# Optimization experiments

Measured on AMD Instinct MI355X. Metric: run time of the kernel, lower is better.

## Reference

```python
import jax, jax.numpy as jnp
import numpy as np

EPS = 1e-7  # Keras backend epsilon


def setup_inputs() -> dict:
    key = jax.random.key(0)
    kx, ka, ke, kp = jax.random.split(key, 4)
    B, N, F, K_, C = 8, 2048, 128, 128, 128
    X = jax.random.normal(kx, (B, N, F), dtype=jnp.float32)
    Au = (jax.random.uniform(ka, (B, N, N)) < 0.05).astype(jnp.float32)
    A = jnp.maximum(Au, jnp.swapaxes(Au, -1, -2))
    W_emb = jax.random.normal(ke, (F, C), dtype=jnp.float32) * 0.1
    W_pool = jax.random.normal(kp, (F, K_), dtype=jnp.float32) * 0.1
    return {"X": X, "A": A, "W_emb": W_emb, "W_pool": W_pool}


def _diffpool(X, A, W_emb, W_pool):
    N = A.shape[-1]
    I = jnp.eye(N, dtype=A.dtype)
    A_ = A + I
    # symmetric normalization D^-1/2 (A+I) D^-1/2
    d = jax.lax.rsqrt(jnp.sum(A_, axis=-1))          # [B, N]
    fltr = A_ * d[..., :, None] * d[..., None, :]    # [B, N, N]

    Z = jnp.einsum('bnm,bmc->bnc', fltr, X @ W_emb)  # embedding GNN (no activation)
    S = jax.nn.softmax(jnp.einsum('bnm,bmk->bnk', fltr, X @ W_pool), axis=-1)  # [B, N, k]

    # link prediction loss: ||A - S S^T||_F per graph, mean over batch
    S_gram = jnp.einsum('bnk,bmk->bnm', S, S)
    LP_loss = jnp.mean(jnp.linalg.norm(A - S_gram, ord='fro', axis=(-1, -2)))

    # entropy loss on assignments
    entr = -jnp.sum(S * jnp.log(S + EPS), axis=-1)   # [B, N]
    entr_loss = jnp.mean(entr)

    X_pooled = jnp.einsum('bnk,bnc->bkc', S, Z)                  # S^T Z
    A_pooled = jnp.einsum('bnk,bnm,bml->bkl', S, A, S)           # S^T A S
    return X_pooled, A_pooled, S, LP_loss, entr_loss


def reference(X, A, W_emb, W_pool):
    return _diffpool(X, A, W_emb, W_pool)
```

## Files before the change

### kernel.cpp

```cpp
#include <hip/hip_runtime.h>
#include <math.h>

typedef __bf16 bf16x8 __attribute__((ext_vector_type(8)));
typedef float  f32x4  __attribute__((ext_vector_type(4)));
typedef unsigned short u16x4 __attribute__((ext_vector_type(4)));

#define DEVI __device__ __forceinline__

static constexpr int NB  = 8;
static constexpr int NN  = 2048;
static constexpr int NF  = 128;
static constexpr int NC2 = 256;

static constexpr int OUT_X0  = 0;
static constexpr int OUT_A0  = NB * 128 * 128;
static constexpr int OUT_S0  = OUT_A0 + NB * 128 * 128;
static constexpr int OUT_LP  = OUT_S0 + NB * NN * 128;
static constexpr int OUT_ENT = OUT_LP + 1;

DEVI unsigned short f2b(float f) {
  unsigned int u = __builtin_bit_cast(unsigned int, f);
  u += 0x7fffu + ((u >> 16) & 1u);
  return (unsigned short)(u >> 16);
}
DEVI float b2f(unsigned short h) {
  unsigned int u = ((unsigned int)h) << 16;
  return __builtin_bit_cast(float, u);
}
DEVI void load_lds16(const void* g, void* l) {
  __builtin_amdgcn_global_load_lds(
      (const __attribute__((address_space(1))) void*)g,
      (__attribute__((address_space(3))) void*)l, 16, 0, 0);
}

DEVI void stage_tile(const unsigned short* src, int ld, unsigned short* dst,
                     int k0, int tid) {
  const int wave = tid >> 6;
#pragma unroll
  for (int is = 0; is < 2; ++is) {
    const int row = is * 64 + (tid >> 2);
    const int c   = tid & 3;
    const unsigned short* g = src + row * ld + k0 + ((c ^ (row & 3)) << 3);
    unsigned short* l = dst + ((is * 256 + wave * 64) << 3);
    load_lds16(g, l);
  }
}

DEVI void gemm_core(const unsigned short* Aop, int lda,
                    const unsigned short* Bop, int ldb, int ksteps,
                    unsigned short* lA0, unsigned short* lA1,
                    unsigned short* lB0, unsigned short* lB1,
                    int tid, f32x4 (&acc)[4][4]) {
  const int lane = tid & 63;
  const int wave = tid >> 6;
  const int wr = wave >> 1, wc = wave & 1;
  const int l15 = lane & 15;
  const int sx = (lane >> 4) ^ (l15 & 3);
#pragma unroll
  for (int i = 0; i < 4; ++i) {
#pragma unroll
    for (int j = 0; j < 4; ++j) acc[i][j] = (f32x4){0.f, 0.f, 0.f, 0.f};
  }
  stage_tile(Aop, lda, lA0, 0, tid);
  stage_tile(Bop, ldb, lB0, 0, tid);
  __syncthreads();
  for (int kt = 0; kt < ksteps; ++kt) {
    unsigned short* curA = (kt & 1) ? lA1 : lA0;
    unsigned short* curB = (kt & 1) ? lB1 : lB0;
    if (kt + 1 < ksteps) {
      unsigned short* nxtA = (kt & 1) ? lA0 : lA1;
      unsigned short* nxtB = (kt & 1) ? lB0 : lB1;
      stage_tile(Aop, lda, nxtA, (kt + 1) * 32, tid);
      stage_tile(Bop, ldb, nxtB, (kt + 1) * 32, tid);
    }
    bf16x8 af[4], bg[4];
#pragma unroll
    for (int i = 0; i < 4; ++i) {
      const int row = wr * 64 + i * 16 + l15;
      af[i] = *(const bf16x8*)(curA + ((row * 4 + sx) << 3));
    }
#pragma unroll
    for (int j = 0; j < 4; ++j) {
      const int col = wc * 64 + j * 16 + l15;
      bg[j] = *(const bf16x8*)(curB + ((col * 4 + sx) << 3));
    }
#pragma unroll
    for (int i = 0; i < 4; ++i) {
#pragma unroll
      for (int j = 0; j < 4; ++j)
        acc[i][j] = __builtin_amdgcn_mfma_f32_16x16x32_bf16(af[i], bg[j],
                                                            acc[i][j], 0, 0, 0);
    }
    __syncthreads();
  }
}


__global__ __launch_bounds__(256) void k_prep_a(const float* __restrict__ A,
                                                unsigned short* __restrict__ AB,
                                                float* __restrict__ dvec,
                                                float* __restrict__ rsum) {
  const int row = blockIdx.x * 4 + (threadIdx.x >> 6);
  const int lane = threadIdx.x & 63;
  const f32x4* src = (const f32x4*)(A + ((size_t)row << 11));
  u16x4* dst = (u16x4*)(AB + ((size_t)row << 11));
  float s = 0.f;
#pragma unroll
  for (int it = 0; it < 8; ++it) {
    f32x4 v = src[it * 64 + lane];
    s += v[0] + v[1] + v[2] + v[3];
    u16x4 o;
    o[0] = f2b(v[0]); o[1] = f2b(v[1]); o[2] = f2b(v[2]); o[3] = f2b(v[3]);
    dst[it * 64 + lane] = o;
  }
#pragma unroll
  for (int o2 = 32; o2; o2 >>= 1) s += __shfl_down(s, o2);
  if (lane == 0) {
    dvec[row] = rsqrtf(s + 1.f);
    rsum[row] = s;
  }
}

__global__ __launch_bounds__(256) void k_conv_x(const float* __restrict__ X,
                                                unsigned short* __restrict__ XB) {
  const int i0 = blockIdx.x * 1024 + threadIdx.x;
  const f32x4* src = (const f32x4*)X;
  u16x4* dst = (u16x4*)XB;
#pragma unroll
  for (int it = 0; it < 4; ++it) {
    const int idx = i0 + it * 256;
    f32x4 v = src[idx];
    u16x4 o;
    o[0] = f2b(v[0]); o[1] = f2b(v[1]); o[2] = f2b(v[2]); o[3] = f2b(v[3]);
    dst[idx] = o;
  }
}

__global__ __launch_bounds__(128) void k_prep_w(const float* __restrict__ Wemb,
                                                const float* __restrict__ Wpool,
                                                unsigned short* __restrict__ WT) {
  const int c = blockIdx.x, f = threadIdx.x;
  const float v = (c < 128) ? Wemb[f * 128 + c] : Wpool[f * 128 + (c - 128)];
  WT[c * 128 + f] = f2b(v);
}

__global__ __launch_bounds__(256) void k_gemm_xw(const unsigned short* __restrict__ XB,
                                                 const unsigned short* __restrict__ WT,
                                                 const float* __restrict__ dvec,
                                                 unsigned short* __restrict__ VT) {
  __shared__ unsigned short lA[2][4096], lB[2][4096];
  const int mt = blockIdx.x, ct = blockIdx.y, tid = threadIdx.x;
  f32x4 acc[4][4];
  gemm_core(XB + mt * 128 * NF, NF, WT + ct * 128 * NF, NF, NF / 32,
            lA[0], lA[1], lB[0], lB[1], tid, acc);
  const int lane = tid & 63, wave = tid >> 6;
  const int wr = wave >> 1, wc = wave & 1, l15 = lane & 15, l4 = (lane >> 4) * 4;
#pragma unroll
  for (int i = 0; i < 4; ++i) {
    const int gr0 = mt * 128 + wr * 64 + i * 16 + l4;
    const int b = gr0 >> 11, n0 = gr0 & 2047;
#pragma unroll
    for (int j = 0; j < 4; ++j) {
      const int gc = ct * 128 + wc * 64 + j * 16 + l15;
      u16x4 pk;
#pragma unroll
      for (int r = 0; r < 4; ++r) pk[r] = f2b(acc[i][j][r] * dvec[gr0 + r]);
      *(u16x4*)(VT + (((size_t)(b * NC2 + gc)) << 11) + n0) = pk;
    }
  }
}

__global__ __launch_bounds__(256) void k_gemm_nv(const unsigned short* __restrict__ AB,
                                                 const unsigned short* __restrict__ VT,
                                                 const float* __restrict__ dvec,
                                                 unsigned short* YT, float* SpT) {
  __shared__ unsigned short lA[2][4096], lB[2][4096];
  const int mt = blockIdx.x, ct = blockIdx.y, b = blockIdx.z, tid = threadIdx.x;
  const unsigned short* Aop = AB + ((size_t)b << 22) + (size_t)mt * 128 * NN;
  const unsigned short* Bop = VT + (((size_t)(b * NC2 + ct * 128)) << 11);
  f32x4 acc[4][4];
  gemm_core(Aop, NN, Bop, NN, NN / 32, lA[0], lA[1], lB[0], lB[1], tid, acc);
  const int lane = tid & 63, wave = tid >> 6;
  const int wr = wave >> 1, wc = wave & 1, l15 = lane & 15, l4 = (lane >> 4) * 4;
#pragma unroll
  for (int i = 0; i < 4; ++i) {
    const int n0 = mt * 128 + wr * 64 + i * 16 + l4;
#pragma unroll
    for (int j = 0; j < 4; ++j) {
      const int c = ct * 128 + wc * 64 + j * 16 + l15;
      const unsigned short* vt = VT + (((size_t)(b * NC2 + c)) << 11);
      if (ct == 0) {
        u16x4 pk;
#pragma unroll
        for (int r = 0; r < 4; ++r)
          pk[r] = f2b((acc[i][j][r] + b2f(vt[n0 + r])) * dvec[(b << 11) + n0 + r]);
        *(u16x4*)(YT + (((size_t)(b * 384 + c)) << 11) + n0) = pk;
      } else {
        f32x4 pk;
#pragma unroll
        for (int r = 0; r < 4; ++r)
          pk[r] = (acc[i][j][r] + b2f(vt[n0 + r])) * dvec[(b << 11) + n0 + r];
        *(f32x4*)(SpT + (((size_t)(b * 128 + (c - 128))) << 11) + n0) = pk;
      }
    }
  }
}

__global__ __launch_bounds__(128) void k_softmax(const float* __restrict__ SpT,
                                                 float* __restrict__ out,
                                                 unsigned short* __restrict__ YT,
                                                 float* __restrict__ entv) {
  const int t = blockIdx.x, b = blockIdx.y;
  const int tid = threadIdx.x;
  const int h = tid >> 6, r = tid & 63;
  const int n = t * 64 + r;
  const float* src = SpT + (((size_t)(b * 128 + h * 64)) << 11) + n;
  float x[64];
  float m = -1e30f;
#pragma unroll
  for (int k = 0; k < 64; ++k) { x[k] = src[(size_t)k << 11]; m = fmaxf(m, x[k]); }
  __shared__ float smx[2][64], sms[2][64], smt[2][64];
  smx[h][r] = m;
  __syncthreads();
  m = fmaxf(smx[0][r], smx[1][r]);
  float s = 0.f, tt = 0.f;
#pragma unroll
  for (int k = 0; k < 64; ++k) {
    const float e = __expf(x[k] - m);
    s += e; tt += (x[k] - m) * e; x[k] = e;
  }
  sms[h][r] = s; smt[h][r] = tt;
  __syncthreads();
  s = sms[0][r] + sms[1][r];
  tt = smt[0][r] + smt[1][r];
  const float inv = 1.f / s;
  float* po = out + OUT_S0 + (((size_t)(b * NN + n)) << 7) + h * 64;
#pragma unroll
  for (int k4 = 0; k4 < 16; ++k4) {
    f32x4 v;
    v[0] = x[k4*4+0]*inv; v[1] = x[k4*4+1]*inv; v[2] = x[k4*4+2]*inv; v[3] = x[k4*4+3]*inv;
    *(f32x4*)(po + k4 * 4) = v;
  }
  unsigned short* pt = YT + (((size_t)(b * 384 + 256 + h * 64)) << 11) + n;
#pragma unroll
  for (int k = 0; k < 64; ++k) pt[(size_t)k << 11] = f2b(x[k] * inv);
  if (h == 0) {
    float entr = __logf(s) - tt * inv;
#pragma unroll
    for (int o2 = 32; o2; o2 >>= 1) entr += __shfl_down(entr, o2);
    if (tid == 0) entv[b * 32 + t] = entr;
  }
}

__global__ __launch_bounds__(256) void k_gemm_as(const unsigned short* __restrict__ AB,
                                                 unsigned short* YT) {
  __shared__ unsigned short lA[2][4096], lB[2][4096];
  const int mt = blockIdx.x, b = blockIdx.z, tid = threadIdx.x;
  const unsigned short* Aop = AB + ((size_t)b << 22) + (size_t)mt * 128 * NN;
  const unsigned short* Bop = YT + (((size_t)(b * 384 + 256)) << 11);
  f32x4 acc[4][4];
  gemm_core(Aop, NN, Bop, NN, NN / 32, lA[0], lA[1], lB[0], lB[1], tid, acc);
  const int lane = tid & 63, wave = tid >> 6;
  const int wr = wave >> 1, wc = wave & 1, l15 = lane & 15, l4 = (lane >> 4) * 4;
#pragma unroll
  for (int i = 0; i < 4; ++i) {
    const int n0 = mt * 128 + wr * 64 + i * 16 + l4;
#pragma unroll
    for (int j = 0; j < 4; ++j) {
      const int c = wc * 64 + j * 16 + l15;
      u16x4 pk;
#pragma unroll
      for (int r = 0; r < 4; ++r) pk[r] = f2b(acc[i][j][r]);
      *(u16x4*)(YT + (((size_t)(b * 384 + 128 + c)) << 11) + n0) = pk;
    }
  }
}

__global__ __launch_bounds__(256) void k_gemm_p(const unsigned short* __restrict__ YT,
                                                float* __restrict__ Pp) {
  __shared__ unsigned short lA[2][4096], lB[2][4096];
  const int ct = blockIdx.x, sk = blockIdx.y, b = blockIdx.z, tid = threadIdx.x;
  const unsigned short* Aop = YT + (((size_t)(b * 384 + 256)) << 11) + sk * 256;
  const unsigned short* Bop = YT + (((size_t)(b * 384 + ct * 128)) << 11) + sk * 256;
  f32x4 acc[4][4];
  gemm_core(Aop, NN, Bop, NN, 8, lA[0], lA[1], lB[0], lB[1], tid, acc);
  const int lane = tid & 63, wave = tid >> 6;
  const int wr = wave >> 1, wc = wave & 1, l15 = lane & 15, l4 = (lane >> 4) * 4;
  float* dst = Pp + ((size_t)(sk * NB + b)) * 128 * 384;
#pragma unroll
  for (int i = 0; i < 4; ++i) {
    const int p0 = wr * 64 + i * 16 + l4;
#pragma unroll
    for (int j = 0; j < 4; ++j) {
      const int gc = ct * 128 + wc * 64 + j * 16 + l15;
#pragma unroll
      for (int r = 0; r < 4; ++r) dst[(p0 + r) * 384 + gc] = acc[i][j][r];
    }
  }
}

__global__ __launch_bounds__(256) void k_reduce_p(const float* __restrict__ Pp,
                                                  float* __restrict__ trp,
                                                  float* __restrict__ g2p,
                                                  float* __restrict__ out) {
  const int chunk = blockIdx.x, b = blockIdx.y, tid = threadIdx.x;
  const int e = chunk * 256 + tid;
  const int p = e / 384, c = e - p * 384;
  float s = 0.f;
#pragma unroll
  for (int sk = 0; sk < 8; ++sk)
    s += Pp[((size_t)(sk * NB + b)) * (128 * 384) + e];
  float tr = 0.f, g2 = 0.f;
  if (c < 128) {
    out[OUT_X0 + ((size_t)(b * 128 + p)) * 128 + c] = s;
  } else if (c < 256) {
    out[OUT_A0 + ((size_t)(b * 128 + p)) * 128 + (c - 128)] = s;
    if (c - 128 == p) tr = s;
  } else {
    g2 = s * s;
  }
  __shared__ float rb[512];
  rb[tid] = tr; rb[256 + tid] = g2;
  __syncthreads();
  for (int o = 128; o; o >>= 1) {
    if (tid < o) { rb[tid] += rb[tid + o]; rb[256 + tid] += rb[256 + tid + o]; }
    __syncthreads();
  }
  if (tid == 0) { trp[b * 192 + chunk] = rb[0]; g2p[b * 192 + chunk] = rb[256]; }
}

__global__ __launch_bounds__(256) void k_lp(const float* __restrict__ rsum,
                                            const float* __restrict__ trp,
                                            const float* __restrict__ g2p,
                                            float* __restrict__ lpv) {
  const int b = blockIdx.x, tid = threadIdx.x;
  float nz = 0.f;
#pragma unroll
  for (int i = 0; i < 8; ++i) nz += rsum[(b << 11) + i * 256 + tid];
  float tr = (tid < 192) ? trp[b * 192 + tid] : 0.f;
  float g2 = (tid < 192) ? g2p[b * 192 + tid] : 0.f;
  __shared__ float rb[768];
  rb[tid] = nz; rb[256 + tid] = tr; rb[512 + tid] = g2;
  __syncthreads();
  for (int o = 128; o; o >>= 1) {
    if (tid < o) {
      rb[tid] += rb[tid + o];
      rb[256 + tid] += rb[256 + tid + o];
      rb[512 + tid] += rb[512 + tid + o];
    }
    __syncthreads();
  }
  if (tid == 0)
    lpv[b] = sqrtf(fmaxf(rb[0] - 2.f * rb[256] + rb[512], 0.f));
}

__global__ __launch_bounds__(256) void k_losses(const float* __restrict__ entv,
                                                const float* __restrict__ lpv,
                                                float* __restrict__ out) {
  const int tid = threadIdx.x;
  __shared__ float rb[256];
  rb[tid] = entv[tid];
  __syncthreads();
  for (int o = 128; o; o >>= 1) {
    if (tid < o) rb[tid] += rb[tid + o];
    __syncthreads();
  }
  if (tid == 0) {
    float lp = 0.f;
#pragma unroll
    for (int b = 0; b < 8; ++b) lp += lpv[b];
    out[OUT_LP] = 0.125f * lp;
    out[OUT_ENT] = rb[0] * (1.f / (NB * NN));
  }
}

extern "C" void kernel_launch(void* const* d_in, const int* in_sizes, int n_in,
                              void* d_out, int out_size, void* d_ws, size_t ws_size,
                              hipStream_t stream) {
  const float* X     = (const float*)d_in[0];
  const float* A     = (const float*)d_in[1];
  const float* Wemb  = (const float*)d_in[2];
  const float* Wpool = (const float*)d_in[3];
  float* out = (float*)d_out;

  char* ws = (char*)d_ws;
  size_t o = 0;
  unsigned short* AB = (unsigned short*)(ws + o); o += (size_t)NB * NN * NN * 2;
  unsigned short* XB = (unsigned short*)(ws + o); o += (size_t)NB * NN * NF * 2;
  unsigned short* WT = (unsigned short*)(ws + o); o += (size_t)NC2 * NF * 2;
  unsigned short* VT = (unsigned short*)(ws + o); o += (size_t)NB * NC2 * NN * 2;
  unsigned short* YT = (unsigned short*)(ws + o); o += (size_t)NB * 384 * NN * 2;
  float* SpT = (float*)(ws + o); o += (size_t)NB * 128 * NN * 4;
  float* Pp  = (float*)(ws + o); o += (size_t)8 * NB * 128 * 384 * 4;
  float* dvec = (float*)(ws + o); o += (size_t)NB * NN * 4;
  float* rsum = (float*)(ws + o); o += (size_t)NB * NN * 4;
  float* trp  = (float*)(ws + o); o += (size_t)NB * 192 * 4;
  float* g2p  = (float*)(ws + o); o += (size_t)NB * 192 * 4;
  float* entv = (float*)(ws + o); o += 256 * 4;
  float* lpv  = (float*)(ws + o); o += NB * 4;

  k_prep_a  <<<dim3(NB * NN / 4), 256, 0, stream>>>(A, AB, dvec, rsum);
  k_conv_x  <<<dim3(512), 256, 0, stream>>>(X, XB);
  k_prep_w  <<<dim3(NC2), 128, 0, stream>>>(Wemb, Wpool, WT);
  k_gemm_xw <<<dim3(NB * NN / 128, 2), 256, 0, stream>>>(XB, WT, dvec, VT);
  k_gemm_nv <<<dim3(NN / 128, 2, NB), 256, 0, stream>>>(AB, VT, dvec, YT, SpT);
  k_softmax <<<dim3(NN / 64, NB), 128, 0, stream>>>(SpT, out, YT, entv);
  k_gemm_as <<<dim3(NN / 128, 1, NB), 256, 0, stream>>>(AB, YT);
  k_gemm_p  <<<dim3(3, 8, NB), 256, 0, stream>>>(YT, Pp);
  k_reduce_p<<<dim3(192, NB), 256, 0, stream>>>(Pp, trp, g2p, out);
  k_lp      <<<dim3(NB), 256, 0, stream>>>(rsum, trp, g2p, lpv);
  k_losses  <<<1, 256, 0, stream>>>(entv, lpv, out);
}
```

Baseline: 330.6 us.

## Fuse softmax and entropy into GEMM epilogue, retile A·S GEMM, merge prep kernels

The softmax over pooling logits and the entropy partial sums now run inside the epilogue of the fltr·V GEMM, with LDS reductions across waves. This removes the fp32 SpT intermediate and the separate softmax launch. The A·S GEMM uses 64-row tiles, doubling its block count to fill more CUs, and the X and W conversion kernels are merged into one launch. dvec loads are vectorised. The trade-off is that S is written to the output with strided scalar stores instead of contiguous vector stores, and the epilogue now carries extra syncs and register pressure.

```diff
diff --git a/kernel.cpp b/kernel.cpp
--- a/kernel.cpp
+++ b/kernel.cpp
@@ -121,27 +121,33 @@
   }
 }
 
-__global__ __launch_bounds__(256) void k_conv_x(const float* __restrict__ X,
-                                                unsigned short* __restrict__ XB) {
-  const int i0 = blockIdx.x * 1024 + threadIdx.x;
-  const f32x4* src = (const f32x4*)X;
-  u16x4* dst = (u16x4*)XB;
-#pragma unroll
-  for (int it = 0; it < 4; ++it) {
-    const int idx = i0 + it * 256;
-    f32x4 v = src[idx];
-    u16x4 o;
-    o[0] = f2b(v[0]); o[1] = f2b(v[1]); o[2] = f2b(v[2]); o[3] = f2b(v[3]);
-    dst[idx] = o;
-  }
-}
-
-__global__ __launch_bounds__(128) void k_prep_w(const float* __restrict__ Wemb,
-                                                const float* __restrict__ Wpool,
-                                                unsigned short* __restrict__ WT) {
-  const int c = blockIdx.x, f = threadIdx.x;
-  const float v = (c < 128) ? Wemb[f * 128 + c] : Wpool[f * 128 + (c - 128)];
-  WT[c * 128 + f] = f2b(v);
+__global__ __launch_bounds__(256) void k_conv_xw(const float* __restrict__ X,
+                                                 const float* __restrict__ Wemb,
+                                                 const float* __restrict__ Wpool,
+                                                 unsigned short* __restrict__ XB,
+                                                 unsigned short* __restrict__ WT) {
+  const int blk = blockIdx.x, tid = threadIdx.x;
+  if (blk < 512) {
+    const int i0 = blk * 1024 + tid;
+    const f32x4* src = (const f32x4*)X;
+    u16x4* dst = (u16x4*)XB;
+#pragma unroll
+    for (int it = 0; it < 4; ++it) {
+      const int idx = i0 + it * 256;
+      f32x4 v = src[idx];
+      u16x4 o;
+      o[0] = f2b(v[0]); o[1] = f2b(v[1]); o[2] = f2b(v[2]); o[3] = f2b(v[3]);
+      dst[idx] = o;
+    }
+  } else {
+    const int e = (blk - 512) * 256 + tid;
+    const int c = e >> 4, f0 = (e & 15) * 8;
+    const float* W = (c < 128) ? Wemb : Wpool;
+    const int cc = c & 127;
+#pragma unroll
+    for (int q = 0; q < 8; ++q)
+      WT[c * 128 + f0 + q] = f2b(W[(f0 + q) * 128 + cc]);
+  }
 }
 
 __global__ __launch_bounds__(256) void k_gemm_xw(const unsigned short* __restrict__ XB,
@@ -159,12 +165,13 @@
   for (int i = 0; i < 4; ++i) {
     const int gr0 = mt * 128 + wr * 64 + i * 16 + l4;
     const int b = gr0 >> 11, n0 = gr0 & 2047;
+    const f32x4 dv = *(const f32x4*)(dvec + gr0);
 #pragma unroll
     for (int j = 0; j < 4; ++j) {
       const int gc = ct * 128 + wc * 64 + j * 16 + l15;
       u16x4 pk;
 #pragma unroll
-      for (int r = 0; r < 4; ++r) pk[r] = f2b(acc[i][j][r] * dvec[gr0 + r]);
+      for (int r = 0; r < 4; ++r) pk[r] = f2b(acc[i][j][r] * dv[r]);
       *(u16x4*)(VT + (((size_t)(b * NC2 + gc)) << 11) + n0) = pk;
     }
   }
@@ -173,7 +180,9 @@
 __global__ __launch_bounds__(256) void k_gemm_nv(const unsigned short* __restrict__ AB,
                                                  const unsigned short* __restrict__ VT,
                                                  const float* __restrict__ dvec,
-                                                 unsigned short* YT, float* SpT) {
+                                                 unsigned short* __restrict__ YT,
+                                                 float* __restrict__ out,
+                                                 float* __restrict__ entv) {
   __shared__ unsigned short lA[2][4096], lB[2][4096];
   const int mt = blockIdx.x, ct = blockIdx.y, b = blockIdx.z, tid = threadIdx.x;
   const unsigned short* Aop = AB + ((size_t)b << 22) + (size_t)mt * 128 * NN;
@@ -181,93 +190,187 @@
   f32x4 acc[4][4];
   gemm_core(Aop, NN, Bop, NN, NN / 32, lA[0], lA[1], lB[0], lB[1], tid, acc);
   const int lane = tid & 63, wave = tid >> 6;
-  const int wr = wave >> 1, wc = wave & 1, l15 = lane & 15, l4 = (lane >> 4) * 4;
+  const int wr = wave >> 1, wc = wave & 1, l15 = lane & 15, l4g = lane >> 4;
+  const int l4 = l4g * 4;
+  f32x4 dv[4];
+#pragma unroll
+  for (int i = 0; i < 4; ++i) {
+    const int n0 = mt * 128 + wr * 64 + i * 16 + l4;
+    dv[i] = *(const f32x4*)(dvec + (b << 11) + n0);
+  }
 #pragma unroll
   for (int i = 0; i < 4; ++i) {
     const int n0 = mt * 128 + wr * 64 + i * 16 + l4;
 #pragma unroll
     for (int j = 0; j < 4; ++j) {
       const int c = ct * 128 + wc * 64 + j * 16 + l15;
-      const unsigned short* vt = VT + (((size_t)(b * NC2 + c)) << 11);
-      if (ct == 0) {
+      const u16x4 vv = *(const u16x4*)(VT + (((size_t)(b * NC2 + c)) << 11) + n0);
+#pragma unroll
+      for (int r = 0; r < 4; ++r)
+        acc[i][j][r] = (acc[i][j][r] + b2f(vv[r])) * dv[i][r];
+    }
+  }
+  if (ct == 0) {
+#pragma unroll
+    for (int i = 0; i < 4; ++i) {
+      const int n0 = mt * 128 + wr * 64 + i * 16 + l4;
+#pragma unroll
+      for (int j = 0; j < 4; ++j) {
+        const int c = wc * 64 + j * 16 + l15;
         u16x4 pk;
 #pragma unroll
-        for (int r = 0; r < 4; ++r)
-          pk[r] = f2b((acc[i][j][r] + b2f(vt[n0 + r])) * dvec[(b << 11) + n0 + r]);
+        for (int r = 0; r < 4; ++r) pk[r] = f2b(acc[i][j][r]);
         *(u16x4*)(YT + (((size_t)(b * 384 + c)) << 11) + n0) = pk;
-      } else {
-        f32x4 pk;
-#pragma unroll
-        for (int r = 0; r < 4; ++r)
-          pk[r] = (acc[i][j][r] + b2f(vt[n0 + r])) * dvec[(b << 11) + n0 + r];
-        *(f32x4*)(SpT + (((size_t)(b * 128 + (c - 128))) << 11) + n0) = pk;
       }
     }
-  }
-}
-
-__global__ __launch_bounds__(128) void k_softmax(const float* __restrict__ SpT,
-                                                 float* __restrict__ out,
-                                                 unsigned short* __restrict__ YT,
-                                                 float* __restrict__ entv) {
-  const int t = blockIdx.x, b = blockIdx.y;
-  const int tid = threadIdx.x;
-  const int h = tid >> 6, r = tid & 63;
-  const int n = t * 64 + r;
-  const float* src = SpT + (((size_t)(b * 128 + h * 64)) << 11) + n;
-  float x[64];
-  float m = -1e30f;
-#pragma unroll
-  for (int k = 0; k < 64; ++k) { x[k] = src[(size_t)k << 11]; m = fmaxf(m, x[k]); }
-  __shared__ float smx[2][64], sms[2][64], smt[2][64];
-  smx[h][r] = m;
-  __syncthreads();
-  m = fmaxf(smx[0][r], smx[1][r]);
-  float s = 0.f, tt = 0.f;
-#pragma unroll
-  for (int k = 0; k < 64; ++k) {
-    const float e = __expf(x[k] - m);
-    s += e; tt += (x[k] - m) * e; x[k] = e;
-  }
-  sms[h][r] = s; smt[h][r] = tt;
-  __syncthreads();
-  s = sms[0][r] + sms[1][r];
-  tt = smt[0][r] + smt[1][r];
-  const float inv = 1.f / s;
-  float* po = out + OUT_S0 + (((size_t)(b * NN + n)) << 7) + h * 64;
-#pragma unroll
-  for (int k4 = 0; k4 < 16; ++k4) {
-    f32x4 v;
-    v[0] = x[k4*4+0]*inv; v[1] = x[k4*4+1]*inv; v[2] = x[k4*4+2]*inv; v[3] = x[k4*4+3]*inv;
-    *(f32x4*)(po + k4 * 4) = v;
-  }
-  unsigned short* pt = YT + (((size_t)(b * 384 + 256 + h * 64)) << 11) + n;
-#pragma unroll
-  for (int k = 0; k < 64; ++k) pt[(size_t)k << 11] = f2b(x[k] * inv);
-  if (h == 0) {
-    float entr = __logf(s) - tt * inv;
-#pragma unroll
-    for (int o2 = 32; o2; o2 >>= 1) entr += __shfl_down(entr, o2);
-    if (tid == 0) entv[b * 32 + t] = entr;
-  }
-}
-
-__global__ __launch_bounds__(256) void k_gemm_as(const unsigned short* __restrict__ AB,
-                                                 unsigned short* YT) {
-  __shared__ unsigned short lA[2][4096], lB[2][4096];
-  const int mt = blockIdx.x, b = blockIdx.z, tid = threadIdx.x;
-  const unsigned short* Aop = AB + ((size_t)b << 22) + (size_t)mt * 128 * NN;
-  const unsigned short* Bop = YT + (((size_t)(b * 384 + 256)) << 11);
-  f32x4 acc[4][4];
-  gemm_core(Aop, NN, Bop, NN, NN / 32, lA[0], lA[1], lB[0], lB[1], tid, acc);
-  const int lane = tid & 63, wave = tid >> 6;
-  const int wr = wave >> 1, wc = wave & 1, l15 = lane & 15, l4 = (lane >> 4) * 4;
+    return;
+  }
+  float* mbuf = (float*)lA;
+  float* sbuf = mbuf + 256;
+  float* tbuf = mbuf + 512;
+  float* ebuf = mbuf + 768;
+  float rm[4][4], rs[4][4], rt[4][4];
+#pragma unroll
+  for (int i = 0; i < 4; ++i)
+#pragma unroll
+    for (int r = 0; r < 4; ++r) {
+      float m = fmaxf(fmaxf(acc[i][0][r], acc[i][1][r]),
+                      fmaxf(acc[i][2][r], acc[i][3][r]));
+#pragma unroll
+      for (int off = 1; off < 16; off <<= 1) m = fmaxf(m, __shfl_xor(m, off));
+      if (l15 == 0) mbuf[(wr * 2 + wc) * 64 + i * 16 + l4 + r] = m;
+    }
+  __syncthreads();
+#pragma unroll
+  for (int i = 0; i < 4; ++i)
+#pragma unroll
+    for (int r = 0; r < 4; ++r) {
+      const int row = i * 16 + l4 + r;
+      rm[i][r] = fmaxf(mbuf[(wr * 2) * 64 + row], mbuf[(wr * 2 + 1) * 64 + row]);
+      rs[i][r] = 0.f; rt[i][r] = 0.f;
+    }
+#pragma unroll
+  for (int i = 0; i < 4; ++i)
+#pragma unroll
+    for (int j = 0; j < 4; ++j)
+#pragma unroll
+      for (int r = 0; r < 4; ++r) {
+        const float xm = acc[i][j][r] - rm[i][r];
+        const float e = __expf(xm);
+        acc[i][j][r] = e;
+        rs[i][r] += e;
+        rt[i][r] += xm * e;
+      }
+  __syncthreads();
+#pragma unroll
+  for (int i = 0; i < 4; ++i)
+#pragma unroll
+    for (int r = 0; r < 4; ++r) {
+      float s = rs[i][r], t = rt[i][r];
+#pragma unroll
+      for (int off = 1; off < 16; off <<= 1) {
+        s += __shfl_xor(s, off); t += __shfl_xor(t, off);
+      }
+      if (l15 == 0) {
+        sbuf[(wr * 2 + wc) * 64 + i * 16 + l4 + r] = s;
+        tbuf[(wr * 2 + wc) * 64 + i * 16 + l4 + r] = t;
+      }
+    }
+  __syncthreads();
+  float ent = 0.f;
+#pragma unroll
+  for (int i = 0; i < 4; ++i)
+#pragma unroll
+    for (int r = 0; r < 4; ++r) {
+      const int row = i * 16 + l4 + r;
+      const float s = sbuf[(wr * 2) * 64 + row] + sbuf[(wr * 2 + 1) * 64 + row];
+      const float t = tbuf[(wr * 2) * 64 + row] + tbuf[(wr * 2 + 1) * 64 + row];
+      const float inv = 1.f / s;
+      rs[i][r] = inv;
+      ent += __logf(s) - t * inv;
+    }
 #pragma unroll
   for (int i = 0; i < 4; ++i) {
     const int n0 = mt * 128 + wr * 64 + i * 16 + l4;
 #pragma unroll
     for (int j = 0; j < 4; ++j) {
       const int c = wc * 64 + j * 16 + l15;
+      u16x4 pk;
+#pragma unroll
+      for (int r = 0; r < 4; ++r) {
+        const float sv = acc[i][j][r] * rs[i][r];
+        pk[r] = f2b(sv);
+        out[OUT_S0 + (((size_t)((b << 11) + n0 + r)) << 7) + c] = sv;
+      }
+      *(u16x4*)(YT + (((size_t)(b * 384 + 256 + c)) << 11) + n0) = pk;
+    }
+  }
+  if (wc == 0 && l15 == 0) ebuf[wr * 4 + l4g] = ent;
+  __syncthreads();
+  if (tid == 0) {
+    float e8 = 0.f;
+#pragma unroll
+    for (int q = 0; q < 8; ++q) e8 += ebuf[q];
+    entv[b * 16 + mt] = e8;
+  }
+}
+
+__global__ __launch_bounds__(256) void k_gemm_as(const unsigned short* __restrict__ AB,
+                                                 unsigned short* __restrict__ YT) {
+  __shared__ unsigned short lA[2][2048], lB[2][4096];
+  const int mt = blockIdx.x, b = blockIdx.z, tid = threadIdx.x;
+  const unsigned short* Aop = AB + ((size_t)b << 22) + (size_t)mt * 64 * NN;
+  const unsigned short* Bop = YT + (((size_t)(b * 384 + 256)) << 11);
+  const int lane = tid & 63, wave = tid >> 6;
+  const int l15 = lane & 15;
+  const int sx = (lane >> 4) ^ (l15 & 3);
+  f32x4 acc[4][2];
+#pragma unroll
+  for (int i = 0; i < 4; ++i) {
+    acc[i][0] = (f32x4){0.f, 0.f, 0.f, 0.f};
+    acc[i][1] = (f32x4){0.f, 0.f, 0.f, 0.f};
+  }
+  {
+    const int row = tid >> 2, c = tid & 3;
+    load_lds16(Aop + row * NN + ((c ^ (row & 3)) << 3), lA[0] + (wave << 9));
+  }
+  stage_tile(Bop, NN, lB[0], 0, tid);
+  __syncthreads();
+  for (int kt = 0; kt < 64; ++kt) {
+    unsigned short* curA = lA[kt & 1];
+    unsigned short* curB = lB[kt & 1];
+    if (kt + 1 < 64) {
+      const int k0 = (kt + 1) * 32;
+      const int row = tid >> 2, c = tid & 3;
+      load_lds16(Aop + row * NN + k0 + ((c ^ (row & 3)) << 3),
+                 lA[(kt + 1) & 1] + (wave << 9));
+      stage_tile(Bop, NN, lB[(kt + 1) & 1], k0, tid);
+    }
+    bf16x8 af[4], bg[2];
+#pragma unroll
+    for (int i = 0; i < 4; ++i)
+      af[i] = *(const bf16x8*)(curA + (((i * 16 + l15) * 4 + sx) << 3));
+#pragma unroll
+    for (int j = 0; j < 2; ++j) {
+      const int col = wave * 32 + j * 16 + l15;
+      bg[j] = *(const bf16x8*)(curB + ((col * 4 + sx) << 3));
+    }
+#pragma unroll
+    for (int i = 0; i < 4; ++i) {
+#pragma unroll
+      for (int j = 0; j < 2; ++j)
+        acc[i][j] = __builtin_amdgcn_mfma_f32_16x16x32_bf16(af[i], bg[j],
+                                                            acc[i][j], 0, 0, 0);
+    }
+    __syncthreads();
+  }
+  const int l4 = (lane >> 4) * 4;
+#pragma unroll
+  for (int i = 0; i < 4; ++i) {
+    const int n0 = mt * 64 + i * 16 + l4;
+#pragma unroll
+    for (int j = 0; j < 2; ++j) {
+      const int c = wave * 32 + j * 16 + l15;
       u16x4 pk;
 #pragma unroll
       for (int r = 0; r < 4; ++r) pk[r] = f2b(acc[i][j][r]);
@@ -359,7 +462,7 @@
                                                 float* __restrict__ out) {
   const int tid = threadIdx.x;
   __shared__ float rb[256];
-  rb[tid] = entv[tid];
+  rb[tid] = (tid < 128) ? entv[tid] : 0.f;
   __syncthreads();
   for (int o = 128; o; o >>= 1) {
     if (tid < o) rb[tid] += rb[tid + o];
@@ -390,22 +493,19 @@
   unsigned short* WT = (unsigned short*)(ws + o); o += (size_t)NC2 * NF * 2;
   unsigned short* VT = (unsigned short*)(ws + o); o += (size_t)NB * NC2 * NN * 2;
   unsigned short* YT = (unsigned short*)(ws + o); o += (size_t)NB * 384 * NN * 2;
-  float* SpT = (float*)(ws + o); o += (size_t)NB * 128 * NN * 4;
   float* Pp  = (float*)(ws + o); o += (size_t)8 * NB * 128 * 384 * 4;
   float* dvec = (float*)(ws + o); o += (size_t)NB * NN * 4;
   float* rsum = (float*)(ws + o); o += (size_t)NB * NN * 4;
   float* trp  = (float*)(ws + o); o += (size_t)NB * 192 * 4;
   float* g2p  = (float*)(ws + o); o += (size_t)NB * 192 * 4;
-  float* entv = (float*)(ws + o); o += 256 * 4;
+  float* entv = (float*)(ws + o); o += 128 * 4;
   float* lpv  = (float*)(ws + o); o += NB * 4;
 
   k_prep_a  <<<dim3(NB * NN / 4), 256, 0, stream>>>(A, AB, dvec, rsum);
-  k_conv_x  <<<dim3(512), 256, 0, stream>>>(X, XB);
-  k_prep_w  <<<dim3(NC2), 128, 0, stream>>>(Wemb, Wpool, WT);
+  k_conv_xw <<<dim3(528), 256, 0, stream>>>(X, Wemb, Wpool, XB, WT);
   k_gemm_xw <<<dim3(NB * NN / 128, 2), 256, 0, stream>>>(XB, WT, dvec, VT);
-  k_gemm_nv <<<dim3(NN / 128, 2, NB), 256, 0, stream>>>(AB, VT, dvec, YT, SpT);
-  k_softmax <<<dim3(NN / 64, NB), 128, 0, stream>>>(SpT, out, YT, entv);
-  k_gemm_as <<<dim3(NN / 128, 1, NB), 256, 0, stream>>>(AB, YT);
+  k_gemm_nv <<<dim3(NN / 128, 2, NB), 256, 0, stream>>>(AB, VT, dvec, YT, out, entv);
+  k_gemm_as <<<dim3(NN / 64, 1, NB), 256, 0, stream>>>(AB, YT);
   k_gemm_p  <<<dim3(3, 8, NB), 256, 0, stream>>>(YT, Pp);
   k_reduce_p<<<dim3(192, NB), 256, 0, stream>>>(Pp, trp, g2p, out);
   k_lp      <<<dim3(NB), 256, 0, stream>>>(rsum, trp, g2p, lpv);
```

After: 323.5 us. -2.1%, faster.
